# Performance work log

Hardware: AMD Instinct MI355X
Metric: run time of the kernel (lower is better)

The kernel has to match this reference:

```python
import jax, jax.numpy as jnp
import numpy as np

LEVELS = 256
# skimage graycomatrix offsets: row += round(sin(a)*d), col += round(cos(a)*d)
# for d=1, angles [0, pi/4, pi/2, 3pi/4] -> (0,1), (1,1), (1,0), (1,-1)
OFFSETS = ((0, 1), (1, 1), (1, 0), (1, -1))


def setup_inputs() -> dict:
    key = jax.random.key(0)
    image = jax.random.normal(key, (180, 256, 256), dtype=jnp.float32)
    return {"image": image, "index": 2}


def _glcm_counts(img_u8):
    """Gray-level co-occurrence counts, shape [LEVELS, LEVELS, 4] (one per angle)."""
    H, W = img_u8.shape
    mats = []
    for dr, dc in OFFSETS:
        r0, r1 = max(0, -dr), H - max(0, dr)
        c0, c1 = max(0, -dc), W - max(0, dc)
        a = img_u8[r0:r1, c0:c1]
        b = img_u8[r0 + dr:r1 + dr, c0 + dc:c1 + dc]
        code = (a * LEVELS + b).ravel()  # flattened (i,j) pair index
        mats.append(jnp.bincount(code, length=LEVELS * LEVELS).reshape(LEVELS, LEVELS))
    return jnp.stack(mats, axis=-1)


def reference(image, index):
    band = image[index]  # [H, W]
    # exposure.rescale_intensity(out_range=(0,1)) then img_as_ubyte
    lo, hi = band.min(), band.max()
    scaled = (band - lo) / jnp.maximum(hi - lo, jnp.asarray(1e-12, band.dtype))
    u8 = jnp.clip(jnp.round(scaled * 255.0), 0, 255).astype(jnp.int32)
    counts = _glcm_counts(u8).astype(jnp.float32)  # [256, 256, 4]
    var = jnp.var(counts, axis=-1)  # variance over the 4 angles -> [256, 256]
    return jnp.concatenate([image, var[None]], axis=0).astype(jnp.float32)
```

## Files before the change

### kernel.cpp

```cpp
#include <hip/hip_runtime.h>

#define LEVELS 256
#define HH 256
#define WW 256
#define NPIX 65536
#define NIMG 180

__global__ void copy_kernel(const float4* __restrict__ in, float4* __restrict__ out, int n4) {
    int i = blockIdx.x * blockDim.x + threadIdx.x;
    int stride = gridDim.x * blockDim.x;
    for (; i < n4; i += stride) out[i] = in[i];
}

__global__ void minmax_kernel(const float* __restrict__ image,
                              const int* __restrict__ index,
                              float* __restrict__ mm) {
    const float* band = image + (size_t)index[0] * NPIX;
    const float4* b4 = (const float4*)band;
    int tid = threadIdx.x;
    float lo = 3.402823466e38f, hi = -3.402823466e38f;
    for (int i = tid; i < NPIX / 4; i += blockDim.x) {
        float4 v = b4[i];
        lo = fminf(lo, fminf(fminf(v.x, v.y), fminf(v.z, v.w)));
        hi = fmaxf(hi, fmaxf(fmaxf(v.x, v.y), fmaxf(v.z, v.w)));
    }
    for (int o = 32; o > 0; o >>= 1) {
        lo = fminf(lo, __shfl_down(lo, o));
        hi = fmaxf(hi, __shfl_down(hi, o));
    }
    __shared__ float slo[16], shi[16];
    int wave = tid >> 6, lane = tid & 63;
    if (lane == 0) { slo[wave] = lo; shi[wave] = hi; }
    __syncthreads();
    if (tid == 0) {
        int nw = blockDim.x >> 6;
        for (int w = 1; w < nw; ++w) { lo = fminf(lo, slo[w]); hi = fmaxf(hi, shi[w]); }
        mm[0] = lo;
        mm[1] = hi;
    }
}

__global__ void quant_kernel(const float* __restrict__ image,
                             const int* __restrict__ index,
                             const float* __restrict__ mm,
                             unsigned char* __restrict__ codes) {
    int i = blockIdx.x * blockDim.x + threadIdx.x;
    if (i >= NPIX) return;
    const float* band = image + (size_t)index[0] * NPIX;
    float lo = mm[0], hi = mm[1];
    float denom = fmaxf(hi - lo, 1e-12f);
    float s = (band[i] - lo) / denom;
    float v = rintf(s * 255.0f);
    v = fminf(fmaxf(v, 0.0f), 255.0f);
    codes[i] = (unsigned char)v;
}

__global__ void hist_kernel(const unsigned char* __restrict__ codes,
                            unsigned int* __restrict__ hist) {
    int i = blockIdx.x * blockDim.x + threadIdx.x;
    if (i >= NPIX) return;
    int r = i >> 8, c = i & 255;
    int a = codes[i];
    const int drs[4] = {0, 1, 1, 1};
    const int dcs[4] = {1, 1, 0, -1};
#pragma unroll
    for (int k = 0; k < 4; ++k) {
        int rr = r + drs[k], cc = c + dcs[k];
        if (rr < HH && cc >= 0 && cc < WW) {
            int b = codes[(rr << 8) | cc];
            atomicAdd(&hist[k * NPIX + a * LEVELS + b], 1u);
        }
    }
}

__global__ void var_kernel(const unsigned int* __restrict__ hist,
                           float* __restrict__ out_var) {
    int i = blockIdx.x * blockDim.x + threadIdx.x;
    if (i >= NPIX) return;
    float c0 = (float)hist[i];
    float c1 = (float)hist[NPIX + i];
    float c2 = (float)hist[2 * NPIX + i];
    float c3 = (float)hist[3 * NPIX + i];
    float m = (c0 + c1 + c2 + c3) * 0.25f;
    float d0 = c0 - m, d1 = c1 - m, d2 = c2 - m, d3 = c3 - m;
    float var = ((d0 * d0 + d1 * d1) + (d2 * d2 + d3 * d3)) * 0.25f;
    out_var[i] = var;
}

extern "C" void kernel_launch(void* const* d_in, const int* in_sizes, int n_in,
                              void* d_out, int out_size, void* d_ws, size_t ws_size,
                              hipStream_t stream) {
    const float* image = (const float*)d_in[0];
    const int* index = (const int*)d_in[1];
    float* out = (float*)d_out;

    unsigned int* hist = (unsigned int*)d_ws;
    unsigned char* codes = (unsigned char*)d_ws + (size_t)4 * NPIX * sizeof(unsigned int);
    float* mm = (float*)((char*)d_ws + (size_t)4 * NPIX * sizeof(unsigned int) + NPIX);

    hipMemsetAsync(hist, 0, (size_t)4 * NPIX * sizeof(unsigned int), stream);

    int n4 = NIMG * NPIX / 4;
    copy_kernel<<<2048, 256, 0, stream>>>((const float4*)image, (float4*)out, n4);

    minmax_kernel<<<1, 1024, 0, stream>>>(image, index, mm);

    quant_kernel<<<NPIX / 256, 256, 0, stream>>>(image, index, mm, codes);

    hist_kernel<<<NPIX / 256, 256, 0, stream>>>(codes, hist);

    var_kernel<<<NPIX / 256, 256, 0, stream>>>(hist, out + (size_t)NIMG * NPIX);
}
```

Before: 51.56 us.

## Fuse copy, hist zeroing and minmax into one launch; fuse quantize into histogram

Merges the memset, bulk image copy and min/max reduction into a single kernel, with one extra block computing the min/max while the other blocks copy and zero the histogram. Quantization is folded into the histogram kernel, which recomputes the codes of neighbouring pixels instead of reading a stored byte buffer. This cuts five launches plus a memset down to three and drops the codes round trip. In exchange, the min/max block now competes with the copy blocks, and each pixel is quantized up to five times.

```diff
diff --git a/kernel.cpp b/kernel.cpp
--- a/kernel.cpp
+++ b/kernel.cpp
@@ -1,80 +1,91 @@
 #include <hip/hip_runtime.h>
 
 #define LEVELS 256
-#define HH 256
-#define WW 256
 #define NPIX 65536
 #define NIMG 180
+#define COPY_BLOCKS 2048
 
-__global__ void copy_kernel(const float4* __restrict__ in, float4* __restrict__ out, int n4) {
-    int i = blockIdx.x * blockDim.x + threadIdx.x;
-    int stride = gridDim.x * blockDim.x;
-    for (; i < n4; i += stride) out[i] = in[i];
-}
-
-__global__ void minmax_kernel(const float* __restrict__ image,
-                              const int* __restrict__ index,
-                              float* __restrict__ mm) {
-    const float* band = image + (size_t)index[0] * NPIX;
-    const float4* b4 = (const float4*)band;
-    int tid = threadIdx.x;
-    float lo = 3.402823466e38f, hi = -3.402823466e38f;
-    for (int i = tid; i < NPIX / 4; i += blockDim.x) {
-        float4 v = b4[i];
-        lo = fminf(lo, fminf(fminf(v.x, v.y), fminf(v.z, v.w)));
-        hi = fmaxf(hi, fmaxf(fmaxf(v.x, v.y), fmaxf(v.z, v.w)));
-    }
-    for (int o = 32; o > 0; o >>= 1) {
-        lo = fminf(lo, __shfl_down(lo, o));
-        hi = fmaxf(hi, __shfl_down(hi, o));
-    }
-    __shared__ float slo[16], shi[16];
-    int wave = tid >> 6, lane = tid & 63;
-    if (lane == 0) { slo[wave] = lo; shi[wave] = hi; }
-    __syncthreads();
-    if (tid == 0) {
-        int nw = blockDim.x >> 6;
-        for (int w = 1; w < nw; ++w) { lo = fminf(lo, slo[w]); hi = fmaxf(hi, shi[w]); }
-        mm[0] = lo;
-        mm[1] = hi;
-    }
-}
-
-__global__ void quant_kernel(const float* __restrict__ image,
-                             const int* __restrict__ index,
-                             const float* __restrict__ mm,
-                             unsigned char* __restrict__ codes) {
-    int i = blockIdx.x * blockDim.x + threadIdx.x;
-    if (i >= NPIX) return;
-    const float* band = image + (size_t)index[0] * NPIX;
-    float lo = mm[0], hi = mm[1];
-    float denom = fmaxf(hi - lo, 1e-12f);
-    float s = (band[i] - lo) / denom;
-    float v = rintf(s * 255.0f);
-    v = fminf(fmaxf(v, 0.0f), 255.0f);
-    codes[i] = (unsigned char)v;
-}
-
-__global__ void hist_kernel(const unsigned char* __restrict__ codes,
-                            unsigned int* __restrict__ hist) {
-    int i = blockIdx.x * blockDim.x + threadIdx.x;
-    if (i >= NPIX) return;
-    int r = i >> 8, c = i & 255;
-    int a = codes[i];
-    const int drs[4] = {0, 1, 1, 1};
-    const int dcs[4] = {1, 1, 0, -1};
-#pragma unroll
-    for (int k = 0; k < 4; ++k) {
-        int rr = r + drs[k], cc = c + dcs[k];
-        if (rr < HH && cc >= 0 && cc < WW) {
-            int b = codes[(rr << 8) | cc];
-            atomicAdd(&hist[k * NPIX + a * LEVELS + b], 1u);
+__global__ void k1_copy_zero_minmax(const float* __restrict__ image,
+                                    const int* __restrict__ index,
+                                    float* __restrict__ out,
+                                    unsigned int* __restrict__ hist,
+                                    float* __restrict__ mm) {
+    if (blockIdx.x < COPY_BLOCKS) {
+        int gid = blockIdx.x * blockDim.x + threadIdx.x;
+        if (gid < NPIX) {
+            ((uint4*)hist)[gid] = make_uint4(0u, 0u, 0u, 0u);
+        }
+        const float4* in4 = (const float4*)image;
+        float4* out4 = (float4*)out;
+        const int n4 = NIMG * NPIX / 4;
+        const int stride = COPY_BLOCKS * 256;
+        for (int i = gid; i < n4; i += stride) out4[i] = in4[i];
+    } else {
+        const float* band = image + (size_t)index[0] * NPIX;
+        const float4* b4 = (const float4*)band;
+        int tid = threadIdx.x;
+        float lo = 3.402823466e38f, hi = -3.402823466e38f;
+        for (int i = tid; i < NPIX / 4; i += 256) {
+            float4 v = b4[i];
+            lo = fminf(lo, fminf(fminf(v.x, v.y), fminf(v.z, v.w)));
+            hi = fmaxf(hi, fmaxf(fmaxf(v.x, v.y), fmaxf(v.z, v.w)));
+        }
+        for (int o = 32; o > 0; o >>= 1) {
+            lo = fminf(lo, __shfl_down(lo, o));
+            hi = fmaxf(hi, __shfl_down(hi, o));
+        }
+        __shared__ float slo[4], shi[4];
+        int wave = tid >> 6, lane = tid & 63;
+        if (lane == 0) { slo[wave] = lo; shi[wave] = hi; }
+        __syncthreads();
+        if (tid == 0) {
+            for (int w = 1; w < 4; ++w) { lo = fminf(lo, slo[w]); hi = fmaxf(hi, shi[w]); }
+            mm[0] = lo;
+            mm[1] = hi;
         }
     }
 }
 
-__global__ void var_kernel(const unsigned int* __restrict__ hist,
-                           float* __restrict__ out_var) {
+__device__ __forceinline__ int quant_code(const float* band, int j, float lo, float denom) {
+    float s = (band[j] - lo) / denom;
+    float v = rintf(s * 255.0f);
+    v = fminf(fmaxf(v, 0.0f), 255.0f);
+    return (int)v;
+}
+
+__global__ void k2_hist(const float* __restrict__ image,
+                        const int* __restrict__ index,
+                        const float* __restrict__ mm,
+                        unsigned int* __restrict__ hist) {
+    int i = blockIdx.x * blockDim.x + threadIdx.x;
+    if (i >= NPIX) return;
+    const float* band = image + (size_t)index[0] * NPIX;
+    float lo = mm[0];
+    float denom = fmaxf(mm[1] - lo, 1e-12f);
+    int r = i >> 8, c = i & 255;
+    int a = quant_code(band, i, lo, denom);
+    if (c + 1 < 256) {
+        int b = quant_code(band, i + 1, lo, denom);
+        atomicAdd(&hist[0 * NPIX + a * LEVELS + b], 1u);
+    }
+    if (r + 1 < 256) {
+        if (c + 1 < 256) {
+            int b = quant_code(band, i + 257, lo, denom);
+            atomicAdd(&hist[1 * NPIX + a * LEVELS + b], 1u);
+        }
+        {
+            int b = quant_code(band, i + 256, lo, denom);
+            atomicAdd(&hist[2 * NPIX + a * LEVELS + b], 1u);
+        }
+        if (c - 1 >= 0) {
+            int b = quant_code(band, i + 255, lo, denom);
+            atomicAdd(&hist[3 * NPIX + a * LEVELS + b], 1u);
+        }
+    }
+}
+
+__global__ void k3_var(const unsigned int* __restrict__ hist,
+                       float* __restrict__ out_var) {
     int i = blockIdx.x * blockDim.x + threadIdx.x;
     if (i >= NPIX) return;
     float c0 = (float)hist[i];
@@ -83,8 +94,7 @@
     float c3 = (float)hist[3 * NPIX + i];
     float m = (c0 + c1 + c2 + c3) * 0.25f;
     float d0 = c0 - m, d1 = c1 - m, d2 = c2 - m, d3 = c3 - m;
-    float var = ((d0 * d0 + d1 * d1) + (d2 * d2 + d3 * d3)) * 0.25f;
-    out_var[i] = var;
+    out_var[i] = ((d0 * d0 + d1 * d1) + (d2 * d2 + d3 * d3)) * 0.25f;
 }
 
 extern "C" void kernel_launch(void* const* d_in, const int* in_sizes, int n_in,
@@ -95,19 +105,11 @@
     float* out = (float*)d_out;
 
     unsigned int* hist = (unsigned int*)d_ws;
-    unsigned char* codes = (unsigned char*)d_ws + (size_t)4 * NPIX * sizeof(unsigned int);
-    float* mm = (float*)((char*)d_ws + (size_t)4 * NPIX * sizeof(unsigned int) + NPIX);
+    float* mm = (float*)((char*)d_ws + (size_t)4 * NPIX * sizeof(unsigned int));
 
-    hipMemsetAsync(hist, 0, (size_t)4 * NPIX * sizeof(unsigned int), stream);
+    k1_copy_zero_minmax<<<COPY_BLOCKS + 1, 256, 0, stream>>>(image, index, out, hist, mm);
 
-    int n4 = NIMG * NPIX / 4;
-    copy_kernel<<<2048, 256, 0, stream>>>((const float4*)image, (float4*)out, n4);
+    k2_hist<<<NPIX / 256, 256, 0, stream>>>(image, index, mm, hist);
 
-    minmax_kernel<<<1, 1024, 0, stream>>>(image, index, mm);
-
-    quant_kernel<<<NPIX / 256, 256, 0, stream>>>(image, index, mm, codes);
-
-    hist_kernel<<<NPIX / 256, 256, 0, stream>>>(codes, hist);
-
-    var_kernel<<<NPIX / 256, 256, 0, stream>>>(hist, out + (size_t)NIMG * NPIX);
+    k3_var<<<NPIX / 256, 256, 0, stream>>>(hist, out + (size_t)NIMG * NPIX);
 }
```

New measurement: 50.52 us. -2.0%, faster.
